# Kernel tuning notes

Hardware: AMD Instinct MI355X
Metric: run time of the kernel (lower is better)

The kernel has to match this reference:

```python
import jax, jax.numpy as jnp
import numpy as np

D_MODEL = 512
H = 8
D_K = D_MODEL // H


def setup_inputs() -> dict:
    key = jax.random.key(0)
    ks = jax.random.split(key, 11)
    B, S = 2, 2048
    scale = 1.0 / np.sqrt(D_MODEL)
    return {
        "q": jax.random.normal(ks[0], (B, S, D_MODEL), jnp.float32),
        "v": jax.random.normal(ks[1], (B, S, D_MODEL), jnp.float32),
        "k": jax.random.normal(ks[2], (B, S, D_MODEL), jnp.float32),
        "w_q": jax.random.normal(ks[3], (D_MODEL, D_MODEL), jnp.float32) * scale,
        "b_q": jnp.zeros((D_MODEL,), jnp.float32),
        "w_k": jax.random.normal(ks[4], (D_MODEL, D_MODEL), jnp.float32) * scale,
        "b_k": jnp.zeros((D_MODEL,), jnp.float32),
        "w_v": jax.random.normal(ks[5], (D_MODEL, D_MODEL), jnp.float32) * scale,
        "b_v": jnp.zeros((D_MODEL,), jnp.float32),
        "w_o": jax.random.normal(ks[6], (D_MODEL, D_MODEL), jnp.float32) * scale,
        "b_o": jnp.zeros((D_MODEL,), jnp.float32),
    }


def reference(q, v, k, w_q, b_q, w_k, b_k, w_v, b_v, w_o, b_o):
    B, S, _ = q.shape
    # projections (nn.Linear: x @ W.T + b)
    query = q @ w_q.T + b_q
    key_t = k @ w_k.T + b_k
    value = v @ w_v.T + b_v
    # split heads: [B, S, H, D_K] -> [B, H, S, D_K]
    query = query.reshape(B, S, H, D_K).transpose(0, 2, 1, 3)
    key_t = key_t.reshape(B, S, H, D_K).transpose(0, 2, 1, 3)
    value = value.reshape(B, S, H, D_K).transpose(0, 2, 1, 3)
    # unfused attention: full [B, H, S, S] score matrix
    scores = jnp.einsum("bhqd,bhkd->bhqk", query, key_t) / jnp.sqrt(
        jnp.asarray(D_K, query.dtype)
    )
    attn = jax.nn.softmax(scores, axis=-1)  # dropout inactive in eval
    x = jnp.einsum("bhqk,bhkd->bhqd", attn, value)
    # merge heads and output projection
    x = x.transpose(0, 2, 1, 3).reshape(B, S, D_MODEL)
    return x @ w_o.T + b_o
```

## Files before the change

### kernel.cpp

```cpp
#include <hip/hip_runtime.h>
#include <hip/hip_bf16.h>


typedef __attribute__((ext_vector_type(8))) short short8;
typedef __attribute__((ext_vector_type(4))) short short4v;
typedef __attribute__((ext_vector_type(4))) float f32x4;

#define DM 512
#define SEQ 2048
#define NROW 4096

__device__ __forceinline__ short f2bf_bits(float f) {
    __hip_bfloat16 h = __float2bfloat16(f);
    union { __hip_bfloat16 h; short s; } u; u.h = h; return u.s;
}
__device__ __forceinline__ float bf_bits2f(short s) {
    union { short s; __hip_bfloat16 h; } u; u.s = s; return __bfloat162float(u.h);
}

template <int CTRL>
__device__ __forceinline__ float dpp_rot(float x) {
    int i = __builtin_bit_cast(int, x);
    int r = __builtin_amdgcn_update_dpp(i, i, CTRL, 0xF, 0xF, false);
    return __builtin_bit_cast(float, r);
}
__device__ __forceinline__ float rowmax16(float mx) {
    mx = fmaxf(mx, dpp_rot<0x121>(mx));
    mx = fmaxf(mx, dpp_rot<0x122>(mx));
    mx = fmaxf(mx, dpp_rot<0x124>(mx));
    mx = fmaxf(mx, dpp_rot<0x128>(mx));
    return mx;
}

__device__ __forceinline__ void gload_lds16(const void* src, void* lds_dst) {
    __builtin_amdgcn_global_load_lds(
        (const __attribute__((address_space(1))) unsigned int*)src,
        (__attribute__((address_space(3))) unsigned int*)lds_dst, 16, 0, 0);
}

__device__ __forceinline__ void stage64(const short* __restrict__ gsrc, size_t gstride,
                                        short* lds, int wave, int lane) {
    #pragma unroll
    for (int i = 0; i < 2; i++) {
        const int g   = (i * 4 + wave) * 64 + lane;
        const int row = g >> 3;
        const int cb  = (g & 7) ^ (row & 7);
        gload_lds16(gsrc + (size_t)row * gstride + cb * 8,
                    lds + (size_t)(i * 4 + wave) * 512);
    }
}

__global__ void detect_dtype(const unsigned int* __restrict__ q, int* __restrict__ flag) {
    __shared__ int cnt;
    if (threadIdx.x == 0) cnt = 0;
    __syncthreads();
    int local = 0;
    for (int i = threadIdx.x; i < 1024; i += 256) {
        unsigned int lo = q[i] & 0x7FFFu;
        if (lo >= 0x3000u && lo < 0x4400u) local++;
    }
    atomicAdd(&cnt, local);
    __syncthreads();
    if (threadIdx.x == 0) *flag = (cnt < 512) ? 1 : 0;
}

struct ConvArgs { const void* src[11]; short* dst[11]; int n[11]; };
__global__ void convert_all(ConvArgs a, const int* __restrict__ flag) {
    const bool f32m = (*flag != 0);
    const int tid = blockIdx.x * 256 + threadIdx.x;
    const int stride = gridDim.x * 256;
    if (f32m) {
        for (int s = 0; s < 11; s++) {
            const float4* sp = (const float4*)a.src[s];
            short4v* dp = (short4v*)a.dst[s];
            const int n4 = a.n[s] >> 2;
            for (int i = tid; i < n4; i += stride) {
                float4 v = sp[i];
                short4v o;
                o[0] = f2bf_bits(v.x); o[1] = f2bf_bits(v.y);
                o[2] = f2bf_bits(v.z); o[3] = f2bf_bits(v.w);
                dp[i] = o;
            }
        }
    } else {
        for (int s = 0; s < 11; s++) {
            const short4v* sp = (const short4v*)a.src[s];
            short4v* dp = (short4v*)a.dst[s];
            const int n4 = a.n[s] >> 2;
            for (int i = tid; i < n4; i += stride) dp[i] = sp[i];
        }
    }
}

__device__ __forceinline__ void gemm_core(const short* __restrict__ A,
                                          const short* __restrict__ W,
                                          int m0, int n0,
                                          short* Alds, short* Blds,
                                          int wave, int lane, f32x4 acc[4]) {
    const int rc = lane & 15, quad = lane >> 4;
    const int arow = wave * 16 + rc;
    for (int k0 = 0; k0 < DM; k0 += 64) {
        __syncthreads();
        stage64(A + (size_t)m0 * DM + k0, DM, Alds, wave, lane);
        stage64(W + (size_t)n0 * DM + k0, DM, Blds, wave, lane);
        __builtin_amdgcn_s_waitcnt(0x3F70);
        __syncthreads();
        #pragma unroll
        for (int h = 0; h < 2; h++) {
            short8 af = *(const short8*)&Alds[arow * 64 + (((quad + 4 * h) ^ (arow & 7)) * 8)];
            #pragma unroll
            for (int nt = 0; nt < 4; nt++) {
                const int brow = nt * 16 + rc;
                short8 bf = *(const short8*)&Blds[brow * 64 + (((quad + 4 * h) ^ (brow & 7)) * 8)];
                acc[nt] = __builtin_amdgcn_mfma_f32_16x16x32_bf16(af, bf, acc[nt], 0, 0, 0);
            }
        }
    }
}

struct QKVArgs {
    const short* A[3]; const short* W[3]; const short* Bi[3];
    short* Cq; short* Ck; short* Cv;
};
__global__ __launch_bounds__(256, 4) void qkv_gemm(QKVArgs args) {
    __shared__ __align__(16) short Alds[64 * 64];
    __shared__ __align__(16) short Blds[64 * 64];
    const int z = blockIdx.z;
    const int wave = threadIdx.x >> 6, lane = threadIdx.x & 63;
    const int rc = lane & 15, quad = lane >> 4;
    const int m0 = blockIdx.x * 64, n0 = blockIdx.y * 64;

    f32x4 acc[4];
    #pragma unroll
    for (int nt = 0; nt < 4; nt++) acc[nt] = f32x4{0.f, 0.f, 0.f, 0.f};
    gemm_core(args.A[z], args.W[z], m0, n0, Alds, Blds, wave, lane, acc);

    const short* bias = args.Bi[z];
    const int mw = m0 + wave * 16;
    if (z == 2) {
        short* Vt = args.Cv;
        const int hh = n0 >> 6;
        const int b = mw >> 11;
        const int sbase = mw & 2047;
        #pragma unroll
        for (int nt = 0; nt < 4; nt++) {
            const int d = nt * 16 + rc;
            const float bv = bf_bits2f(bias[n0 + d]);
            short4v pk;
            #pragma unroll
            for (int r = 0; r < 4; r++) pk[r] = f2bf_bits(acc[nt][r] + bv);
            *(short4v*)(Vt + ((size_t)((b * 8 + hh) * 64 + d)) * SEQ + sbase + quad * 4) = pk;
        }
    } else {
        short* C = (z == 0) ? args.Cq : args.Ck;
        const float qs = (z == 0) ? 0.125f : 1.0f;
        #pragma unroll
        for (int nt = 0; nt < 4; nt++) {
            const int col = n0 + nt * 16 + rc;
            const float bv = bf_bits2f(bias[col]);
            #pragma unroll
            for (int r = 0; r < 4; r++)
                C[(size_t)(mw + quad * 4 + r) * DM + col] = f2bf_bits((acc[nt][r] + bv) * qs);
        }
    }
}

__global__ __launch_bounds__(256, 4) void out_gemm(
    const short* __restrict__ A, const short* __restrict__ W,
    const short* __restrict__ bias, void* __restrict__ Cout,
    const int* __restrict__ flag) {
    __shared__ __align__(16) short Alds[64 * 64];
    __shared__ __align__(16) short Blds[64 * 64];
    const int wave = threadIdx.x >> 6, lane = threadIdx.x & 63;
    const int rc = lane & 15, quad = lane >> 4;
    const int m0 = blockIdx.x * 64, n0 = blockIdx.y * 64;
    f32x4 acc[4];
    #pragma unroll
    for (int nt = 0; nt < 4; nt++) acc[nt] = f32x4{0.f, 0.f, 0.f, 0.f};
    gemm_core(A, W, m0, n0, Alds, Blds, wave, lane, acc);
    const bool f32out = (*flag != 0);
    const int mw = m0 + wave * 16;
    #pragma unroll
    for (int nt = 0; nt < 4; nt++) {
        const int col = n0 + nt * 16 + rc;
        const float bv = bf_bits2f(bias[col]);
        #pragma unroll
        for (int r = 0; r < 4; r++) {
            const size_t idx = (size_t)(mw + quad * 4 + r) * DM + col;
            const float val = acc[nt][r] + bv;
            if (f32out) ((float*)Cout)[idx] = val;
            else        ((short*)Cout)[idx] = f2bf_bits(val);
        }
    }
}

__global__ __launch_bounds__(256, 2) void attn_kernel(
    const short* __restrict__ Q, const short* __restrict__ K,
    const short* __restrict__ Vt, short* __restrict__ O)
{
    __shared__ __align__(16) short Klds[2][64 * 64];
    __shared__ __align__(16) short Vlds[2][64 * 64];
    __shared__ __align__(16) short Plds[4][16 * 72];

    const int wave = threadIdx.x >> 6, lane = threadIdx.x & 63;
    const int rc = lane & 15, quad = lane >> 4;
    const int bh = blockIdx.y;
    const size_t baseQ = (size_t)(bh >> 3) * SEQ * DM + (size_t)(bh & 7) * 64;
    const short* Qb = Q + baseQ;
    const short* Kb = K + baseQ;
    const short* Vb = Vt + (size_t)bh * 64 * SEQ;
    const int q0 = blockIdx.x * 64 + wave * 16;

    short8 qa0 = *(const short8*)(Qb + (size_t)(q0 + rc) * DM + quad * 8);
    short8 qa1 = *(const short8*)(Qb + (size_t)(q0 + rc) * DM + 32 + quad * 8);

    short8 ones;
    #pragma unroll
    for (int j = 0; j < 8; j++) ones[j] = (short)0x3F80;

    f32x4 o[4];
    #pragma unroll
    for (int dt = 0; dt < 4; dt++) o[dt] = f32x4{0.f, 0.f, 0.f, 0.f};
    float mrow[4], lrow[4];
    #pragma unroll
    for (int r = 0; r < 4; r++) { mrow[r] = -1e30f; lrow[r] = 0.f; }
    short* Pw = &Plds[wave][0];

    stage64(Kb, DM, &Klds[0][0], wave, lane);
    stage64(Vb, SEQ, &Vlds[0][0], wave, lane);

    const int NIT = SEQ / 64;
    for (int it = 0; it < NIT; it++) {
        const int cur = it & 1;
        if (it + 1 < NIT) {
            const int k0n = (it + 1) * 64;
            stage64(Kb + (size_t)k0n * DM, DM, &Klds[1 - cur][0], wave, lane);
            stage64(Vb + k0n, SEQ, &Vlds[1 - cur][0], wave, lane);
            __builtin_amdgcn_s_waitcnt(0x3F74);
        } else {
            __builtin_amdgcn_s_waitcnt(0x3F70);
        }
        __asm__ __volatile__("" ::: "memory");
        __builtin_amdgcn_s_barrier();
        __asm__ __volatile__("" ::: "memory");

        const short* Kt = &Klds[cur][0];
        const short* Vtl = &Vlds[cur][0];

        f32x4 s[4];
        #pragma unroll
        for (int kt = 0; kt < 4; kt++) {
            const int row = rc * 4 + kt;
            short8 kf0 = *(const short8*)&Kt[row * 64 + ((quad ^ (row & 7)) * 8)];
            short8 kf1 = *(const short8*)&Kt[row * 64 + (((quad + 4) ^ (row & 7)) * 8)];
            s[kt] = f32x4{0.f, 0.f, 0.f, 0.f};
            s[kt] = __builtin_amdgcn_mfma_f32_16x16x32_bf16(qa0, kf0, s[kt], 0, 0, 0);
            s[kt] = __builtin_amdgcn_mfma_f32_16x16x32_bf16(qa1, kf1, s[kt], 0, 0, 0);
        }
        float alpha[4];
        #pragma unroll
        for (int r = 0; r < 4; r++) {
            float mx = fmaxf(fmaxf(s[0][r], s[1][r]), fmaxf(s[2][r], s[3][r]));
            mx = rowmax16(mx);
            const float mnew = fmaxf(mrow[r], mx);
            alpha[r] = __expf(mrow[r] - mnew);
            mrow[r] = mnew;
            short4v pk;
            #pragma unroll
            for (int kt = 0; kt < 4; kt++) pk[kt] = f2bf_bits(__expf(s[kt][r] - mnew));
            *(short4v*)(&Pw[(quad * 4 + r) * 72 + rc * 4]) = pk;
        }
        #pragma unroll
        for (int dt = 0; dt < 4; dt++)
            #pragma unroll
            for (int r = 0; r < 4; r++) o[dt][r] *= alpha[r];

        __builtin_amdgcn_s_waitcnt(0xC07F);
        short8 pa0 = *(const short8*)(&Pw[rc * 72 + quad * 8]);
        short8 pa1 = *(const short8*)(&Pw[rc * 72 + 32 + quad * 8]);

        f32x4 psum = f32x4{0.f, 0.f, 0.f, 0.f};
        psum = __builtin_amdgcn_mfma_f32_16x16x32_bf16(pa0, ones, psum, 0, 0, 0);
        psum = __builtin_amdgcn_mfma_f32_16x16x32_bf16(pa1, ones, psum, 0, 0, 0);
        #pragma unroll
        for (int dt = 0; dt < 4; dt++) {
            const int row = dt * 16 + rc;
            short8 vv0 = *(const short8*)&Vtl[row * 64 + ((quad ^ (row & 7)) * 8)];
            short8 vv1 = *(const short8*)&Vtl[row * 64 + (((quad + 4) ^ (row & 7)) * 8)];
            o[dt] = __builtin_amdgcn_mfma_f32_16x16x32_bf16(pa0, vv0, o[dt], 0, 0, 0);
            o[dt] = __builtin_amdgcn_mfma_f32_16x16x32_bf16(pa1, vv1, o[dt], 0, 0, 0);
        }
        #pragma unroll
        for (int r = 0; r < 4; r++) lrow[r] = lrow[r] * alpha[r] + psum[r];

        __asm__ __volatile__("" ::: "memory");
        __builtin_amdgcn_s_barrier();
        __asm__ __volatile__("" ::: "memory");
    }

    float inv[4];
    #pragma unroll
    for (int r = 0; r < 4; r++) inv[r] = 1.0f / lrow[r];
    #pragma unroll
    for (int dt = 0; dt < 4; dt++)
        #pragma unroll
        for (int r = 0; r < 4; r++)
            O[baseQ + (size_t)(q0 + quad * 4 + r) * DM + dt * 16 + rc] = f2bf_bits(o[dt][r] * inv[r]);
}

extern "C" void kernel_launch(void* const* d_in, const int* in_sizes, int n_in,
                              void* d_out, int out_size, void* d_ws, size_t ws_size,
                              hipStream_t stream) {
    char* ws = (char*)d_ws;
    const size_t SEQB = (size_t)NROW * DM * sizeof(short);
    const size_t WB   = (size_t)DM * DM * sizeof(short);
    const size_t BB   = (size_t)DM * sizeof(short);

    int* flag = (int*)ws;
    size_t off = 256;
    short* qc = (short*)(ws + off); off += SEQB;
    short* vc = (short*)(ws + off); off += SEQB;
    short* kc = (short*)(ws + off); off += SEQB;
    short* wq = (short*)(ws + off); off += WB;
    short* wk = (short*)(ws + off); off += WB;
    short* wv = (short*)(ws + off); off += WB;
    short* wo = (short*)(ws + off); off += WB;
    short* bq = (short*)(ws + off); off += BB;
    short* bk = (short*)(ws + off); off += BB;
    short* bv = (short*)(ws + off); off += BB;
    short* bo = (short*)(ws + off); off += BB;
    off = (off + 255) & ~(size_t)255;
    short* Qp  = (short*)(ws + off); off += SEQB;
    short* Kp  = (short*)(ws + off); off += SEQB;
    short* Vtp = (short*)(ws + off); off += SEQB;
    short* Xp  = (short*)(ws + off); off += SEQB;

    detect_dtype<<<1, 256, 0, stream>>>((const unsigned int*)d_in[0], flag);

    ConvArgs ca;
    const void* srcs[11] = {d_in[0], d_in[1], d_in[2], d_in[3], d_in[5], d_in[7],
                            d_in[9], d_in[4], d_in[6], d_in[8], d_in[10]};
    short* dsts[11] = {qc, vc, kc, wq, wk, wv, wo, bq, bk, bv, bo};
    int ns[11] = {NROW * DM, NROW * DM, NROW * DM, DM * DM, DM * DM, DM * DM,
                  DM * DM, DM, DM, DM, DM};
    for (int i = 0; i < 11; i++) { ca.src[i] = srcs[i]; ca.dst[i] = dsts[i]; ca.n[i] = ns[i]; }
    convert_all<<<1024, 256, 0, stream>>>(ca, flag);

    QKVArgs qa;
    qa.A[0] = qc; qa.A[1] = kc; qa.A[2] = vc;
    qa.W[0] = wq; qa.W[1] = wk; qa.W[2] = wv;
    qa.Bi[0] = bq; qa.Bi[1] = bk; qa.Bi[2] = bv;
    qa.Cq = Qp; qa.Ck = Kp; qa.Cv = Vtp;
    dim3 gg(NROW / 64, DM / 64, 3);
    qkv_gemm<<<gg, 256, 0, stream>>>(qa);

    dim3 ga(SEQ / 64, 16);
    attn_kernel<<<ga, 256, 0, stream>>>(Qp, Kp, Vtp, Xp);

    dim3 go(NROW / 64, DM / 64);
    out_gemm<<<go, 256, 0, stream>>>(Xp, wo, bo, d_out, flag);
}
```

Measured before the change: 166.4 us.

## Enlarge GEMM and attention tiles, fold dtype detection, use exp2 softmax

The QKV and output GEMMs now compute 128x64 tiles per block, with each wave handling two 16-row M subtiles that reuse the same B fragments. The attention kernel drops to two waves of 32 query rows each. Each wave reuses its K/V LDS fragments across both subtiles, and the loop is unrolled by two over the double buffer. Softmax switches to exp2 with log2e folded into the Q scale, uses bit-trick bf16 rounding with packed stores, and skips the output rescale when no row max changed. The separate dtype-detect launch is folded into the convert and out_gemm kernels, which removes one launch but repeats the detection in every block; halving attention waves per block also risks lower occupancy.

Measured after the change: 195.0 us. 17.2% more time.

```diff
diff --git a/kernel.cpp b/kernel.cpp
--- a/kernel.cpp
+++ b/kernel.cpp
@@ -5,17 +5,32 @@
 typedef __attribute__((ext_vector_type(8))) short short8;
 typedef __attribute__((ext_vector_type(4))) short short4v;
 typedef __attribute__((ext_vector_type(4))) float f32x4;
+typedef __attribute__((ext_vector_type(2))) unsigned int uint2v;
 
 #define DM 512
 #define SEQ 2048
 #define NROW 4096
-
-__device__ __forceinline__ short f2bf_bits(float f) {
-    __hip_bfloat16 h = __float2bfloat16(f);
-    union { __hip_bfloat16 h; short s; } u; u.h = h; return u.s;
-}
+#define LOG2E 1.44269504088896341f
+#define MFMA(a, b, c) __builtin_amdgcn_mfma_f32_16x16x32_bf16(a, b, c, 0, 0, 0)
+
+#if __has_builtin(__builtin_amdgcn_exp2f)
+#define EXP2(x) __builtin_amdgcn_exp2f(x)
+#else
+#define EXP2(x) __expf((x) * 0.6931471805599453f)
+#endif
+
 __device__ __forceinline__ float bf_bits2f(short s) {
-    union { short s; __hip_bfloat16 h; } u; u.s = s; return __bfloat162float(u.h);
+    unsigned int u = ((unsigned int)(unsigned short)s) << 16;
+    return __builtin_bit_cast(float, u);
+}
+__device__ __forceinline__ short f2bf_r(float f) {
+    unsigned int u = __builtin_bit_cast(unsigned int, f) + 0x8000u;
+    return (short)(u >> 16);
+}
+__device__ __forceinline__ unsigned int pack_bf16(float lo, float hi) {
+    unsigned int ul = __builtin_bit_cast(unsigned int, lo) + 0x8000u;
+    unsigned int uh = __builtin_bit_cast(unsigned int, hi) + 0x8000u;
+    return __builtin_amdgcn_perm(uh, ul, 0x07060302u);
 }
 
 template <int CTRL>
@@ -38,35 +53,37 @@
         (__attribute__((address_space(3))) unsigned int*)lds_dst, 16, 0, 0);
 }
 
-__device__ __forceinline__ void stage64(const short* __restrict__ gsrc, size_t gstride,
-                                        short* lds, int wave, int lane) {
-    #pragma unroll
-    for (int i = 0; i < 2; i++) {
-        const int g   = (i * 4 + wave) * 64 + lane;
+template <int ROWS, int NW>
+__device__ __forceinline__ void stage_tile(const short* __restrict__ gsrc, size_t gstride,
+                                           short* lds, int wave, int lane) {
+    constexpr int ISSUES = ROWS * 8 / (64 * NW);
+    #pragma unroll
+    for (int i = 0; i < ISSUES; i++) {
+        const int blk = i * NW + wave;
+        const int g = blk * 64 + lane;
         const int row = g >> 3;
-        const int cb  = (g & 7) ^ (row & 7);
-        gload_lds16(gsrc + (size_t)row * gstride + cb * 8,
-                    lds + (size_t)(i * 4 + wave) * 512);
-    }
-}
-
-__global__ void detect_dtype(const unsigned int* __restrict__ q, int* __restrict__ flag) {
-    __shared__ int cnt;
-    if (threadIdx.x == 0) cnt = 0;
+        const int cb = (g & 7) ^ (row & 7);
+        gload_lds16(gsrc + (size_t)row * gstride + cb * 8, lds + (size_t)blk * 512);
+    }
+}
+
+__device__ __forceinline__ bool detect_f32(const unsigned int* __restrict__ q, int* cnt_lds) {
+    if (threadIdx.x == 0) *cnt_lds = 0;
     __syncthreads();
     int local = 0;
-    for (int i = threadIdx.x; i < 1024; i += 256) {
+    for (int i = threadIdx.x; i < 1024; i += blockDim.x) {
         unsigned int lo = q[i] & 0x7FFFu;
         if (lo >= 0x3000u && lo < 0x4400u) local++;
     }
-    atomicAdd(&cnt, local);
+    if (local) atomicAdd(cnt_lds, local);
     __syncthreads();
-    if (threadIdx.x == 0) *flag = (cnt < 512) ? 1 : 0;
+    return *cnt_lds < 512;
 }
 
 struct ConvArgs { const void* src[11]; short* dst[11]; int n[11]; };
-__global__ void convert_all(ConvArgs a, const int* __restrict__ flag) {
-    const bool f32m = (*flag != 0);
+__global__ void convert_all(ConvArgs a) {
+    __shared__ int cnt;
+    const bool f32m = detect_f32((const unsigned int*)a.src[0], &cnt);
     const int tid = blockIdx.x * 256 + threadIdx.x;
     const int stride = gridDim.x * 256;
     if (f32m) {
@@ -77,8 +94,8 @@
             for (int i = tid; i < n4; i += stride) {
                 float4 v = sp[i];
                 short4v o;
-                o[0] = f2bf_bits(v.x); o[1] = f2bf_bits(v.y);
-                o[2] = f2bf_bits(v.z); o[3] = f2bf_bits(v.w);
+                o[0] = f2bf_r(v.x); o[1] = f2bf_r(v.y);
+                o[2] = f2bf_r(v.z); o[3] = f2bf_r(v.w);
                 dp[i] = o;
             }
         }
@@ -94,25 +111,32 @@
 
 __device__ __forceinline__ void gemm_core(const short* __restrict__ A,
                                           const short* __restrict__ W,
-                                          int m0, int n0,
-                                          short* Alds, short* Blds,
-                                          int wave, int lane, f32x4 acc[4]) {
+                                          int m0, int n0, short* Alds, short* Blds,
+                                          int wave, int lane, f32x4 acc[2][4]) {
     const int rc = lane & 15, quad = lane >> 4;
-    const int arow = wave * 16 + rc;
+    const short* Ag = A + (size_t)m0 * DM;
+    const short* Bg = W + (size_t)n0 * DM;
     for (int k0 = 0; k0 < DM; k0 += 64) {
         __syncthreads();
-        stage64(A + (size_t)m0 * DM + k0, DM, Alds, wave, lane);
-        stage64(W + (size_t)n0 * DM + k0, DM, Blds, wave, lane);
+        stage_tile<128, 4>(Ag + k0, DM, Alds, wave, lane);
+        stage_tile<64, 4>(Bg + k0, DM, Blds, wave, lane);
         __builtin_amdgcn_s_waitcnt(0x3F70);
         __syncthreads();
         #pragma unroll
         for (int h = 0; h < 2; h++) {
-            short8 af = *(const short8*)&Alds[arow * 64 + (((quad + 4 * h) ^ (arow & 7)) * 8)];
+            short8 bf[4];
             #pragma unroll
             for (int nt = 0; nt < 4; nt++) {
-                const int brow = nt * 16 + rc;
-                short8 bf = *(const short8*)&Blds[brow * 64 + (((quad + 4 * h) ^ (brow & 7)) * 8)];
-                acc[nt] = __builtin_amdgcn_mfma_f32_16x16x32_bf16(af, bf, acc[nt], 0, 0, 0);
+                const int br = nt * 16 + rc;
+                bf[nt] = *(const short8*)&Blds[br * 64 + (((quad + 4 * h) ^ (br & 7)) * 8)];
+            }
+            #pragma unroll
+            for (int ms = 0; ms < 2; ms++) {
+                const int ar = wave * 32 + ms * 16 + rc;
+                short8 af = *(const short8*)&Alds[ar * 64 + (((quad + 4 * h) ^ (ar & 7)) * 8)];
+                #pragma unroll
+                for (int nt = 0; nt < 4; nt++)
+                    acc[ms][nt] = MFMA(af, bf[nt], acc[ms][nt]);
             }
         }
     }
@@ -122,85 +146,90 @@
     const short* A[3]; const short* W[3]; const short* Bi[3];
     short* Cq; short* Ck; short* Cv;
 };
-__global__ __launch_bounds__(256, 4) void qkv_gemm(QKVArgs args) {
-    __shared__ __align__(16) short Alds[64 * 64];
+__global__ __launch_bounds__(256, 3) void qkv_gemm(QKVArgs args) {
+    __shared__ __align__(16) short Alds[128 * 64];
     __shared__ __align__(16) short Blds[64 * 64];
     const int z = blockIdx.z;
     const int wave = threadIdx.x >> 6, lane = threadIdx.x & 63;
     const int rc = lane & 15, quad = lane >> 4;
-    const int m0 = blockIdx.x * 64, n0 = blockIdx.y * 64;
-
-    f32x4 acc[4];
-    #pragma unroll
-    for (int nt = 0; nt < 4; nt++) acc[nt] = f32x4{0.f, 0.f, 0.f, 0.f};
+    const int m0 = blockIdx.x * 128, n0 = blockIdx.y * 64;
+
+    f32x4 acc[2][4] = {};
     gemm_core(args.A[z], args.W[z], m0, n0, Alds, Blds, wave, lane, acc);
-
     const short* bias = args.Bi[z];
-    const int mw = m0 + wave * 16;
+
     if (z == 2) {
-        short* Vt = args.Cv;
         const int hh = n0 >> 6;
-        const int b = mw >> 11;
-        const int sbase = mw & 2047;
-        #pragma unroll
-        for (int nt = 0; nt < 4; nt++) {
-            const int d = nt * 16 + rc;
-            const float bv = bf_bits2f(bias[n0 + d]);
-            short4v pk;
-            #pragma unroll
-            for (int r = 0; r < 4; r++) pk[r] = f2bf_bits(acc[nt][r] + bv);
-            *(short4v*)(Vt + ((size_t)((b * 8 + hh) * 64 + d)) * SEQ + sbase + quad * 4) = pk;
+        #pragma unroll
+        for (int ms = 0; ms < 2; ms++) {
+            const int mw = m0 + wave * 32 + ms * 16;
+            const int b = mw >> 11, sb = (mw & 2047) + quad * 4;
+            #pragma unroll
+            for (int nt = 0; nt < 4; nt++) {
+                const int d = nt * 16 + rc;
+                const float bv = bf_bits2f(bias[n0 + d]);
+                short4v pk;
+                #pragma unroll
+                for (int r = 0; r < 4; r++) pk[r] = f2bf_r(acc[ms][nt][r] + bv);
+                *(short4v*)(args.Cv + ((size_t)((b * 8 + hh) * 64 + d)) * SEQ + sb) = pk;
+            }
         }
     } else {
         short* C = (z == 0) ? args.Cq : args.Ck;
-        const float qs = (z == 0) ? 0.125f : 1.0f;
+        const float sc = (z == 0) ? (0.125f * LOG2E) : 1.0f;
+        #pragma unroll
+        for (int ms = 0; ms < 2; ms++) {
+            const int mw = m0 + wave * 32 + ms * 16;
+            #pragma unroll
+            for (int nt = 0; nt < 4; nt++) {
+                const int col = n0 + nt * 16 + rc;
+                const float bv = bf_bits2f(bias[col]);
+                #pragma unroll
+                for (int r = 0; r < 4; r++)
+                    C[(size_t)(mw + quad * 4 + r) * DM + col] = f2bf_r((acc[ms][nt][r] + bv) * sc);
+            }
+        }
+    }
+}
+
+__global__ __launch_bounds__(256, 3) void out_gemm(
+    const short* __restrict__ A, const short* __restrict__ W,
+    const short* __restrict__ bias, void* __restrict__ Cout,
+    const unsigned int* __restrict__ qraw) {
+    __shared__ __align__(16) short Alds[128 * 64];
+    __shared__ __align__(16) short Blds[64 * 64];
+    __shared__ int cnt;
+    const bool f32out = detect_f32(qraw, &cnt);
+    const int wave = threadIdx.x >> 6, lane = threadIdx.x & 63;
+    const int rc = lane & 15, quad = lane >> 4;
+    const int m0 = blockIdx.x * 128, n0 = blockIdx.y * 64;
+    f32x4 acc[2][4] = {};
+    gemm_core(A, W, m0, n0, Alds, Blds, wave, lane, acc);
+    #pragma unroll
+    for (int ms = 0; ms < 2; ms++) {
+        const int mw = m0 + wave * 32 + ms * 16;
         #pragma unroll
         for (int nt = 0; nt < 4; nt++) {
             const int col = n0 + nt * 16 + rc;
             const float bv = bf_bits2f(bias[col]);
             #pragma unroll
-            for (int r = 0; r < 4; r++)
-                C[(size_t)(mw + quad * 4 + r) * DM + col] = f2bf_bits((acc[nt][r] + bv) * qs);
-        }
-    }
-}
-
-__global__ __launch_bounds__(256, 4) void out_gemm(
-    const short* __restrict__ A, const short* __restrict__ W,
-    const short* __restrict__ bias, void* __restrict__ Cout,
-    const int* __restrict__ flag) {
-    __shared__ __align__(16) short Alds[64 * 64];
-    __shared__ __align__(16) short Blds[64 * 64];
-    const int wave = threadIdx.x >> 6, lane = threadIdx.x & 63;
-    const int rc = lane & 15, quad = lane >> 4;
-    const int m0 = blockIdx.x * 64, n0 = blockIdx.y * 64;
-    f32x4 acc[4];
-    #pragma unroll
-    for (int nt = 0; nt < 4; nt++) acc[nt] = f32x4{0.f, 0.f, 0.f, 0.f};
-    gemm_core(A, W, m0, n0, Alds, Blds, wave, lane, acc);
-    const bool f32out = (*flag != 0);
-    const int mw = m0 + wave * 16;
-    #pragma unroll
-    for (int nt = 0; nt < 4; nt++) {
-        const int col = n0 + nt * 16 + rc;
-        const float bv = bf_bits2f(bias[col]);
-        #pragma unroll
-        for (int r = 0; r < 4; r++) {
-            const size_t idx = (size_t)(mw + quad * 4 + r) * DM + col;
-            const float val = acc[nt][r] + bv;
-            if (f32out) ((float*)Cout)[idx] = val;
-            else        ((short*)Cout)[idx] = f2bf_bits(val);
-        }
-    }
-}
-
-__global__ __launch_bounds__(256, 2) void attn_kernel(
+            for (int r = 0; r < 4; r++) {
+                const size_t idx = (size_t)(mw + quad * 4 + r) * DM + col;
+                const float val = acc[ms][nt][r] + bv;
+                if (f32out) ((float*)Cout)[idx] = val;
+                else        ((short*)Cout)[idx] = f2bf_r(val);
+            }
+        }
+    }
+}
+
+__global__ __launch_bounds__(128, 1) void attn_kernel(
     const short* __restrict__ Q, const short* __restrict__ K,
     const short* __restrict__ Vt, short* __restrict__ O)
 {
     __shared__ __align__(16) short Klds[2][64 * 64];
     __shared__ __align__(16) short Vlds[2][64 * 64];
-    __shared__ __align__(16) short Plds[4][16 * 72];
+    __shared__ __align__(16) short Plds[2][2 * 16 * 72];
 
     const int wave = threadIdx.x >> 6, lane = threadIdx.x & 63;
     const int rc = lane & 15, quad = lane >> 4;
@@ -209,34 +238,34 @@
     const short* Qb = Q + baseQ;
     const short* Kb = K + baseQ;
     const short* Vb = Vt + (size_t)bh * 64 * SEQ;
-    const int q0 = blockIdx.x * 64 + wave * 16;
-
-    short8 qa0 = *(const short8*)(Qb + (size_t)(q0 + rc) * DM + quad * 8);
-    short8 qa1 = *(const short8*)(Qb + (size_t)(q0 + rc) * DM + 32 + quad * 8);
+    const int q0 = blockIdx.x * 64 + wave * 32;
+
+    short8 qa[2][2];
+    #pragma unroll
+    for (int ms = 0; ms < 2; ms++)
+        #pragma unroll
+        for (int h = 0; h < 2; h++)
+            qa[ms][h] = *(const short8*)(Qb + (size_t)(q0 + ms * 16 + rc) * DM + h * 32 + quad * 8);
 
     short8 ones;
     #pragma unroll
     for (int j = 0; j < 8; j++) ones[j] = (short)0x3F80;
 
-    f32x4 o[4];
-    #pragma unroll
-    for (int dt = 0; dt < 4; dt++) o[dt] = f32x4{0.f, 0.f, 0.f, 0.f};
-    float mrow[4], lrow[4];
-    #pragma unroll
-    for (int r = 0; r < 4; r++) { mrow[r] = -1e30f; lrow[r] = 0.f; }
+    f32x4 o[2][4] = {};
+    float mrow[8], lrow[8];
+    #pragma unroll
+    for (int i = 0; i < 8; i++) { mrow[i] = -1e30f; lrow[i] = 0.f; }
     short* Pw = &Plds[wave][0];
 
-    stage64(Kb, DM, &Klds[0][0], wave, lane);
-    stage64(Vb, SEQ, &Vlds[0][0], wave, lane);
-
-    const int NIT = SEQ / 64;
-    for (int it = 0; it < NIT; it++) {
-        const int cur = it & 1;
-        if (it + 1 < NIT) {
+    stage_tile<64, 2>(Kb, DM, &Klds[0][0], wave, lane);
+    stage_tile<64, 2>(Vb, SEQ, &Vlds[0][0], wave, lane);
+
+    auto body = [&](int it, int cur) {
+        if (it + 1 < 32) {
             const int k0n = (it + 1) * 64;
-            stage64(Kb + (size_t)k0n * DM, DM, &Klds[1 - cur][0], wave, lane);
-            stage64(Vb + k0n, SEQ, &Vlds[1 - cur][0], wave, lane);
-            __builtin_amdgcn_s_waitcnt(0x3F74);
+            stage_tile<64, 2>(Kb + (size_t)k0n * DM, DM, &Klds[cur ^ 1][0], wave, lane);
+            stage_tile<64, 2>(Vb + k0n, SEQ, &Vlds[cur ^ 1][0], wave, lane);
+            __builtin_amdgcn_s_waitcnt(0x3F78);
         } else {
             __builtin_amdgcn_s_waitcnt(0x3F70);
         }
@@ -245,67 +274,107 @@
         __asm__ __volatile__("" ::: "memory");
 
         const short* Kt = &Klds[cur][0];
-        const short* Vtl = &Vlds[cur][0];
-
-        f32x4 s[4];
+        const short* Vl = &Vlds[cur][0];
+
+        short8 kf[4][2];
         #pragma unroll
         for (int kt = 0; kt < 4; kt++) {
             const int row = rc * 4 + kt;
-            short8 kf0 = *(const short8*)&Kt[row * 64 + ((quad ^ (row & 7)) * 8)];
-            short8 kf1 = *(const short8*)&Kt[row * 64 + (((quad + 4) ^ (row & 7)) * 8)];
-            s[kt] = f32x4{0.f, 0.f, 0.f, 0.f};
-            s[kt] = __builtin_amdgcn_mfma_f32_16x16x32_bf16(qa0, kf0, s[kt], 0, 0, 0);
-            s[kt] = __builtin_amdgcn_mfma_f32_16x16x32_bf16(qa1, kf1, s[kt], 0, 0, 0);
-        }
-        float alpha[4];
-        #pragma unroll
-        for (int r = 0; r < 4; r++) {
-            float mx = fmaxf(fmaxf(s[0][r], s[1][r]), fmaxf(s[2][r], s[3][r]));
-            mx = rowmax16(mx);
-            const float mnew = fmaxf(mrow[r], mx);
-            alpha[r] = __expf(mrow[r] - mnew);
-            mrow[r] = mnew;
-            short4v pk;
-            #pragma unroll
-            for (int kt = 0; kt < 4; kt++) pk[kt] = f2bf_bits(__expf(s[kt][r] - mnew));
-            *(short4v*)(&Pw[(quad * 4 + r) * 72 + rc * 4]) = pk;
-        }
-        #pragma unroll
-        for (int dt = 0; dt < 4; dt++)
-            #pragma unroll
-            for (int r = 0; r < 4; r++) o[dt][r] *= alpha[r];
-
+            #pragma unroll
+            for (int h = 0; h < 2; h++)
+                kf[kt][h] = *(const short8*)&Kt[row * 64 + (((quad + 4 * h) ^ (row & 7)) * 8)];
+        }
+        f32x4 s[2][4];
+        #pragma unroll
+        for (int ms = 0; ms < 2; ms++)
+            #pragma unroll
+            for (int kt = 0; kt < 4; kt++) {
+                f32x4 t = {};
+                t = MFMA(qa[ms][0], kf[kt][0], t);
+                t = MFMA(qa[ms][1], kf[kt][1], t);
+                s[ms][kt] = t;
+            }
+        float alpha[8];
+        #pragma unroll
+        for (int ms = 0; ms < 2; ms++)
+            #pragma unroll
+            for (int r = 0; r < 4; r++) {
+                const float v0 = s[ms][0][r], v1 = s[ms][1][r];
+                const float v2 = s[ms][2][r], v3 = s[ms][3][r];
+                float mx = fmaxf(fmaxf(v0, v1), fmaxf(v2, v3));
+                mx = rowmax16(mx);
+                const int ri = ms * 4 + r;
+                const float mnew = fmaxf(mrow[ri], mx);
+                alpha[ri] = EXP2(mrow[ri] - mnew);
+                mrow[ri] = mnew;
+                uint2v pk;
+                pk[0] = pack_bf16(EXP2(v0 - mnew), EXP2(v1 - mnew));
+                pk[1] = pack_bf16(EXP2(v2 - mnew), EXP2(v3 - mnew));
+                *(uint2v*)(&Pw[(ms * 16 + quad * 4 + r) * 72 + rc * 4]) = pk;
+            }
+        float am = alpha[0];
+        #pragma unroll
+        for (int i = 1; i < 8; i++) am = fminf(am, alpha[i]);
+        if (__ballot(am < 1.0f)) {
+            #pragma unroll
+            for (int ms = 0; ms < 2; ms++)
+                #pragma unroll
+                for (int dt = 0; dt < 4; dt++)
+                    #pragma unroll
+                    for (int r = 0; r < 4; r++)
+                        o[ms][dt][r] *= alpha[ms * 4 + r];
+        }
         __builtin_amdgcn_s_waitcnt(0xC07F);
-        short8 pa0 = *(const short8*)(&Pw[rc * 72 + quad * 8]);
-        short8 pa1 = *(const short8*)(&Pw[rc * 72 + 32 + quad * 8]);
-
-        f32x4 psum = f32x4{0.f, 0.f, 0.f, 0.f};
-        psum = __builtin_amdgcn_mfma_f32_16x16x32_bf16(pa0, ones, psum, 0, 0, 0);
-        psum = __builtin_amdgcn_mfma_f32_16x16x32_bf16(pa1, ones, psum, 0, 0, 0);
+        short8 pa[2][2];
+        #pragma unroll
+        for (int ms = 0; ms < 2; ms++)
+            #pragma unroll
+            for (int h = 0; h < 2; h++)
+                pa[ms][h] = *(const short8*)(&Pw[(ms * 16 + rc) * 72 + h * 32 + quad * 8]);
+        f32x4 psum[2];
+        #pragma unroll
+        for (int ms = 0; ms < 2; ms++) {
+            f32x4 t = {};
+            t = MFMA(pa[ms][0], ones, t);
+            t = MFMA(pa[ms][1], ones, t);
+            psum[ms] = t;
+        }
         #pragma unroll
         for (int dt = 0; dt < 4; dt++) {
             const int row = dt * 16 + rc;
-            short8 vv0 = *(const short8*)&Vtl[row * 64 + ((quad ^ (row & 7)) * 8)];
-            short8 vv1 = *(const short8*)&Vtl[row * 64 + (((quad + 4) ^ (row & 7)) * 8)];
-            o[dt] = __builtin_amdgcn_mfma_f32_16x16x32_bf16(pa0, vv0, o[dt], 0, 0, 0);
-            o[dt] = __builtin_amdgcn_mfma_f32_16x16x32_bf16(pa1, vv1, o[dt], 0, 0, 0);
-        }
-        #pragma unroll
-        for (int r = 0; r < 4; r++) lrow[r] = lrow[r] * alpha[r] + psum[r];
-
+            short8 v0 = *(const short8*)&Vl[row * 64 + ((quad ^ (row & 7)) * 8)];
+            short8 v1 = *(const short8*)&Vl[row * 64 + (((quad + 4) ^ (row & 7)) * 8)];
+            #pragma unroll
+            for (int ms = 0; ms < 2; ms++) {
+                o[ms][dt] = MFMA(pa[ms][0], v0, o[ms][dt]);
+                o[ms][dt] = MFMA(pa[ms][1], v1, o[ms][dt]);
+            }
+        }
+        #pragma unroll
+        for (int i = 0; i < 8; i++)
+            lrow[i] = lrow[i] * alpha[i] + psum[i >> 2][i & 3];
         __asm__ __volatile__("" ::: "memory");
         __builtin_amdgcn_s_barrier();
         __asm__ __volatile__("" ::: "memory");
-    }
-
-    float inv[4];
-    #pragma unroll
-    for (int r = 0; r < 4; r++) inv[r] = 1.0f / lrow[r];
-    #pragma unroll
-    for (int dt = 0; dt < 4; dt++)
-        #pragma unroll
-        for (int r = 0; r < 4; r++)
-            O[baseQ + (size_t)(q0 + quad * 4 + r) * DM + dt * 16 + rc] = f2bf_bits(o[dt][r] * inv[r]);
+    };
+
+    for (int itp = 0; itp < 32; itp += 2) {
+        body(itp, 0);
+        body(itp + 1, 1);
+    }
+
+    #pragma unroll
+    for (int ms = 0; ms < 2; ms++) {
+        float inv[4];
+        #pragma unroll
+        for (int r = 0; r < 4; r++) inv[r] = 1.0f / lrow[ms * 4 + r];
+        #pragma unroll
+        for (int dt = 0; dt < 4; dt++)
+            #pragma unroll
+            for (int r = 0; r < 4; r++)
+                O[baseQ + (size_t)(q0 + ms * 16 + quad * 4 + r) * DM + dt * 16 + rc] =
+                    f2bf_r(o[ms][dt][r] * inv[r]);
+    }
 }
 
 extern "C" void kernel_launch(void* const* d_in, const int* in_sizes, int n_in,
@@ -316,8 +385,7 @@
     const size_t WB   = (size_t)DM * DM * sizeof(short);
     const size_t BB   = (size_t)DM * sizeof(short);
 
-    int* flag = (int*)ws;
-    size_t off = 256;
+    size_t off = 0;
     short* qc = (short*)(ws + off); off += SEQB;
     short* vc = (short*)(ws + off); off += SEQB;
     short* kc = (short*)(ws + off); off += SEQB;
@@ -335,8 +403,6 @@
     short* Vtp = (short*)(ws + off); off += SEQB;
     short* Xp  = (short*)(ws + off); off += SEQB;
 
-    detect_dtype<<<1, 256, 0, stream>>>((const unsigned int*)d_in[0], flag);
-
     ConvArgs ca;
     const void* srcs[11] = {d_in[0], d_in[1], d_in[2], d_in[3], d_in[5], d_in[7],
                             d_in[9], d_in[4], d_in[6], d_in[8], d_in[10]};
@@ -344,19 +410,17 @@
     int ns[11] = {NROW * DM, NROW * DM, NROW * DM, DM * DM, DM * DM, DM * DM,
                   DM * DM, DM, DM, DM, DM};
     for (int i = 0; i < 11; i++) { ca.src[i] = srcs[i]; ca.dst[i] = dsts[i]; ca.n[i] = ns[i]; }
-    convert_all<<<1024, 256, 0, stream>>>(ca, flag);
+    convert_all<<<1024, 256, 0, stream>>>(ca);
 
     QKVArgs qa;
     qa.A[0] = qc; qa.A[1] = kc; qa.A[2] = vc;
     qa.W[0] = wq; qa.W[1] = wk; qa.W[2] = wv;
     qa.Bi[0] = bq; qa.Bi[1] = bk; qa.Bi[2] = bv;
     qa.Cq = Qp; qa.Ck = Kp; qa.Cv = Vtp;
-    dim3 gg(NROW / 64, DM / 64, 3);
-    qkv_gemm<<<gg, 256, 0, stream>>>(qa);
-
-    dim3 ga(SEQ / 64, 16);
-    attn_kernel<<<ga, 256, 0, stream>>>(Qp, Kp, Vtp, Xp);
-
-    dim3 go(NROW / 64, DM / 64);
-    out_gemm<<<go, 256, 0, stream>>>(Xp, wo, bo, d_out, flag);
-}
+    qkv_gemm<<<dim3(NROW / 128, DM / 64, 3), 256, 0, stream>>>(qa);
+
+    attn_kernel<<<dim3(SEQ / 64, 16), 128, 0, stream>>>(Qp, Kp, Vtp, Xp);
+
+    out_gemm<<<dim3(NROW / 128, DM / 64), 256, 0, stream>>>(
+        Xp, wo, bo, d_out, (const unsigned int*)d_in[0]);
+}
```
